# Kernel tuning notes

Hardware: AMD Instinct MI355X
Metric: run time of the kernel (lower is better)

## Reference

```python
import jax, jax.numpy as jnp
import numpy as np

B, S, H = 32, 4096, 512

def setup_inputs() -> dict:
    key = jax.random.key(0)
    k1, k2, k3, k4, k5 = jax.random.split(key, 5)
    scale = 1.0 / np.sqrt(H)
    return {
        "query": jax.random.normal(k1, (B, 1, H), dtype=jnp.float32),
        "keys": jax.random.normal(k2, (B, S, H), dtype=jnp.float32),
        "Wa": jax.random.normal(k3, (H, H), dtype=jnp.float32) * scale,
        "Ua": jax.random.normal(k4, (H, H), dtype=jnp.float32) * scale,
        "Va": jax.random.normal(k5, (H, 1), dtype=jnp.float32) * scale,
    }

def reference(query, keys, Wa, Ua, Va):
    # additive (Bahdanau) attention scores: Va^T tanh(Wa q + Ua k)
    q_proj = jnp.einsum('bqh,hd->bqd', query, Wa)          # [B,1,H]
    k_proj = jnp.einsum('bsh,hd->bsd', keys, Ua)           # [B,S,H]
    scores = jnp.einsum('bsd,d->bs', jnp.tanh(q_proj + k_proj), Va[:, 0])  # [B,S]
    weights = jax.nn.softmax(scores, axis=-1)[:, None, :]  # [B,1,S]
    context = jnp.einsum('bqs,bsh->bqh', weights, keys)    # [B,1,H]
    return (context, weights)
```

## Files before the change

### kernel.cpp

```cpp
#include <hip/hip_runtime.h>
#include <hip/hip_bf16.h>

#define B_ 32
#define S_ 4096
#define H_ 512

typedef short bf16x8 __attribute__((ext_vector_type(8)));
typedef unsigned short u16x8 __attribute__((ext_vector_type(8)));
typedef float f32x4 __attribute__((ext_vector_type(4)));

__device__ inline unsigned short f2bf(float x) {
    unsigned u = __float_as_uint(x);
    return (unsigned short)((u + 0x7fffu + ((u >> 16) & 1u)) >> 16);
}

__device__ inline float fast_tanh(float x) {
    float e = __expf(2.f * x);
    return 1.f - 2.f / (e + 1.f);
}

__device__ __forceinline__ void stage16(const void* g, void* lds_base) {
    __builtin_amdgcn_global_load_lds(
        (const __attribute__((address_space(1))) unsigned char*)g,
        (__attribute__((address_space(3))) unsigned char*)lds_base, 16, 0, 0);
}

__global__ void k_prep_ua(const float* __restrict__ Ua,
                          unsigned short* __restrict__ ua_t) {
    __shared__ float tile[32][33];
    int h0 = blockIdx.x * 32, d0 = blockIdx.y * 32;
    int tx = threadIdx.x, ty = threadIdx.y;
#pragma unroll
    for (int j = 0; j < 4; ++j)
        tile[ty + j * 8][tx] = Ua[(size_t)(h0 + ty + j * 8) * H_ + d0 + tx];
    __syncthreads();
#pragma unroll
    for (int j = 0; j < 4; ++j) {
        int dl = ty + j * 8;
        ua_t[(size_t)(d0 + dl) * H_ + h0 + tx] = f2bf(tile[tx][dl]);
    }
}

__global__ __launch_bounds__(512) void k_qproj(const float* __restrict__ query,
                                               const float* __restrict__ Wa,
                                               float* __restrict__ qproj) {
    __shared__ float q[H_];
    int b = blockIdx.x, d = threadIdx.x;
    q[d] = query[(size_t)b * H_ + d];
    __syncthreads();
    float acc = 0.f;
    for (int h = 0; h < H_; ++h)
        acc = fmaf(q[h], Wa[(size_t)h * H_ + d], acc);
    qproj[(size_t)b * H_ + d] = acc;
}

__global__ __launch_bounds__(256, 3) void k_scores(
    const float* __restrict__ keys, const unsigned short* __restrict__ ua_t,
    const float* __restrict__ qproj, const float* __restrict__ Va,
    float* __restrict__ part_sc) {
    __shared__ __align__(16) unsigned char As[16384];
    __shared__ __align__(16) unsigned char Bs[2][16384];
    __shared__ float smp[2][128];

    int tid = threadIdx.x;
    int wave = tid >> 6, lane = tid & 63;
    int lq = lane & 15, lh = lane >> 4;
    int wm = wave >> 1, wn = wave & 1;

    int logical = (blockIdx.x & 7) * 512 + (blockIdx.x >> 3);
    int b  = logical >> 7;
    int m0 = ((logical >> 2) & 31) * 128;
    int nb = logical & 3;

    const float* keysb = keys + (size_t)b * S_ * H_;

    int r = tid >> 1, hh = tid & 1;
    const float* aptr = keysb + (size_t)(m0 + r) * H_ + hh * 32;
    unsigned aswz = (unsigned)((r & 7) << 4);
    unsigned arow = (unsigned)(r * 128);

    int rbl = lane >> 3;
    unsigned cb = (unsigned)(((lane & 7) * 16) ^ (rbl << 4));
    const unsigned char* uab = (const unsigned char*)ua_t;
    const unsigned char* bsrc[4];
    unsigned bdst[4];
#pragma unroll
    for (int i = 0; i < 4; ++i) {
        int j = wave * 4 + i;
        bsrc[i] = uab + ((size_t)(nb * 128 + 8 * j + rbl)) * 1024 + cb;
        bdst[i] = (unsigned)(j * 1024);
    }

    f32x4 acc[4][4];
#pragma unroll
    for (int i = 0; i < 4; ++i)
#pragma unroll
        for (int j = 0; j < 4; ++j) acc[i][j] = (f32x4){0.f, 0.f, 0.f, 0.f};

#pragma unroll
    for (int i = 0; i < 4; ++i) stage16(bsrc[i], &Bs[0][bdst[i]]);
    {
        float4 a0[8];
#pragma unroll
        for (int j = 0; j < 8; ++j) a0[j] = *(const float4*)(aptr + j * 4);
#pragma unroll
        for (int j16 = 0; j16 < 4; ++j16) {
            float4 x = a0[2 * j16], y = a0[2 * j16 + 1];
            u16x8 v;
            v[0] = f2bf(x.x); v[1] = f2bf(x.y); v[2] = f2bf(x.z); v[3] = f2bf(x.w);
            v[4] = f2bf(y.x); v[5] = f2bf(y.y); v[6] = f2bf(y.z); v[7] = f2bf(y.w);
            *(u16x8*)(As + arow + ((unsigned)(hh * 64 + j16 * 16) ^ aswz)) = v;
        }
    }
    __syncthreads();

#pragma unroll
    for (int t = 0; t < 8; ++t) {
        const int cur = t & 1, nxt = cur ^ 1;
        float4 ar[8];
        if (t < 7) {
#pragma unroll
            for (int i = 0; i < 4; ++i)
                stage16(bsrc[i] + (t + 1) * 128, &Bs[nxt][bdst[i]]);
#pragma unroll
            for (int j = 0; j < 8; ++j)
                ar[j] = *(const float4*)(aptr + (t + 1) * 64 + j * 4);
        }
#pragma unroll
        for (int ks = 0; ks < 2; ++ks) {
            bf16x8 af[4], bv[4];
            unsigned koff = (unsigned)(ks * 64 + lh * 16);
#pragma unroll
            for (int mf = 0; mf < 4; ++mf) {
                unsigned R = (unsigned)(wm * 64 + mf * 16 + lq);
                af[mf] = *(const bf16x8*)(As + R * 128 + (koff ^ ((R & 7) << 4)));
            }
#pragma unroll
            for (int nf = 0; nf < 4; ++nf) {
                unsigned R = (unsigned)(wn * 64 + nf * 16 + lq);
                bv[nf] = *(const bf16x8*)(&Bs[cur][0] + R * 128 + (koff ^ ((R & 7) << 4)));
            }
#pragma unroll
            for (int mf = 0; mf < 4; ++mf)
#pragma unroll
                for (int nf = 0; nf < 4; ++nf)
                    acc[mf][nf] = __builtin_amdgcn_mfma_f32_16x16x32_bf16(
                        af[mf], bv[nf], acc[mf][nf], 0, 0, 0);
        }
        __syncthreads();
        if (t < 7) {
#pragma unroll
            for (int j16 = 0; j16 < 4; ++j16) {
                float4 x = ar[2 * j16], y = ar[2 * j16 + 1];
                u16x8 v;
                v[0] = f2bf(x.x); v[1] = f2bf(x.y); v[2] = f2bf(x.z); v[3] = f2bf(x.w);
                v[4] = f2bf(y.x); v[5] = f2bf(y.y); v[6] = f2bf(y.z); v[7] = f2bf(y.w);
                *(u16x8*)(As + arow + ((unsigned)(hh * 64 + j16 * 16) ^ aswz)) = v;
            }
            __syncthreads();
        }
    }

    float va_r[4], qp_r[4];
#pragma unroll
    for (int nf = 0; nf < 4; ++nf) {
        int n = nb * 128 + wn * 64 + nf * 16 + lq;
        va_r[nf] = Va[n];
        qp_r[nf] = qproj[(size_t)b * H_ + n];
    }
#pragma unroll
    for (int mf = 0; mf < 4; ++mf) {
#pragma unroll
        for (int reg = 0; reg < 4; ++reg) {
            float p = 0.f;
#pragma unroll
            for (int nf = 0; nf < 4; ++nf)
                p += va_r[nf] * fast_tanh(qp_r[nf] + acc[mf][nf][reg]);
            p += __shfl_xor(p, 1);
            p += __shfl_xor(p, 2);
            p += __shfl_xor(p, 4);
            p += __shfl_xor(p, 8);
            if (lq == 0) smp[wn][wm * 64 + mf * 16 + lh * 4 + reg] = p;
        }
    }
    __syncthreads();
    if (tid < 128) {
        float s = smp[0][tid] + smp[1][tid];
        part_sc[((size_t)nb * B_ + b) * S_ + m0 + tid] = s;
    }
}

__global__ __launch_bounds__(512) void k_softmax(const float* __restrict__ part_sc,
                                                 float* __restrict__ wts) {
    __shared__ float red[8];
    int b = blockIdx.x, tid = threadIdx.x;
    const float* p0 = part_sc + (size_t)b * S_;
    const float* p1 = p0 + (size_t)B_ * S_;
    const float* p2 = p1 + (size_t)B_ * S_;
    const float* p3 = p2 + (size_t)B_ * S_;
    float v[8];
    float m = -1e30f;
#pragma unroll
    for (int i = 0; i < 8; ++i) {
        int s = tid + i * 512;
        v[i] = ((p0[s] + p1[s]) + (p2[s] + p3[s]));
        m = fmaxf(m, v[i]);
    }
#pragma unroll
    for (int o = 1; o < 64; o <<= 1) m = fmaxf(m, __shfl_xor(m, o));
    if ((tid & 63) == 0) red[tid >> 6] = m;
    __syncthreads();
    m = red[0];
#pragma unroll
    for (int w = 1; w < 8; ++w) m = fmaxf(m, red[w]);
    float sum = 0.f;
#pragma unroll
    for (int i = 0; i < 8; ++i) {
        v[i] = __expf(v[i] - m);
        sum += v[i];
    }
#pragma unroll
    for (int o = 1; o < 64; o <<= 1) sum += __shfl_xor(sum, o);
    __syncthreads();
    if ((tid & 63) == 0) red[tid >> 6] = sum;
    __syncthreads();
    float tot = 0.f;
#pragma unroll
    for (int w = 0; w < 8; ++w) tot += red[w];
    float inv = 1.f / tot;
#pragma unroll
    for (int i = 0; i < 8; ++i) wts[(size_t)b * S_ + tid + i * 512] = v[i] * inv;
}

__global__ __launch_bounds__(512) void k_ctx_part(const float* __restrict__ keys,
                                                  const float* __restrict__ wts,
                                                  float* __restrict__ part) {
    int c = blockIdx.x, b = blockIdx.y, h = threadIdx.x;
    const float* wrow = wts + (size_t)b * S_ + c * 128;
    const float* kbase = keys + ((size_t)b * S_ + c * 128) * H_ + h;
    float acc = 0.f;
#pragma unroll 8
    for (int s = 0; s < 128; ++s)
        acc = fmaf(wrow[s], kbase[(size_t)s * H_], acc);
    part[((size_t)c * B_ + b) * H_ + h] = acc;
}

__global__ __launch_bounds__(512) void k_ctx_reduce(const float* __restrict__ part,
                                                    float* __restrict__ ctx) {
    int b = blockIdx.x, h = threadIdx.x;
    float s = 0.f;
#pragma unroll
    for (int c = 0; c < 32; ++c) s += part[((size_t)c * B_ + b) * H_ + h];
    ctx[(size_t)b * H_ + h] = s;
}

extern "C" void kernel_launch(void* const* d_in, const int* in_sizes, int n_in,
                              void* d_out, int out_size, void* d_ws, size_t ws_size,
                              hipStream_t stream) {
    const float* query = (const float*)d_in[0];
    const float* keys  = (const float*)d_in[1];
    const float* Wa    = (const float*)d_in[2];
    const float* Ua    = (const float*)d_in[3];
    const float* Va    = (const float*)d_in[4];

    float* out = (float*)d_out;
    float* ctx = out;
    float* wts = out + B_ * H_;

    char* ws = (char*)d_ws;
    unsigned short* ua_t = (unsigned short*)ws;
    float* qproj   = (float*)(ws + 524288);
    float* part_sc = (float*)(ws + 524288 + 65536);
    float* part_cx = (float*)(ws + 524288 + 65536 + 2097152);

    k_prep_ua<<<dim3(16, 16), dim3(32, 8), 0, stream>>>(Ua, ua_t);
    k_qproj<<<dim3(32), dim3(512), 0, stream>>>(query, Wa, qproj);
    k_scores<<<dim3(4096), dim3(256), 0, stream>>>(keys, ua_t, qproj, Va, part_sc);
    k_softmax<<<dim3(32), dim3(512), 0, stream>>>(part_sc, wts);
    k_ctx_part<<<dim3(32, 32), dim3(512), 0, stream>>>(keys, wts, part_cx);
    k_ctx_reduce<<<dim3(32), dim3(512), 0, stream>>>(part_cx, ctx);
}
```

Before: 246.1 us.

## Double-buffer keys tile in LDS and coalesce fp32 key loads

Adds a second LDS buffer for the bf16 keys tile so the next tile is converted and written before the barrier, removing one __syncthreads per k-step. Key loads are remapped so each 16-thread group reads a contiguous 256-byte row segment, and fp32 to bf16 conversion now uses the packed __float22bfloat162_rn intrinsic. The extra 16 KB of LDS lowers the occupancy hint from 3 to 2 blocks per CU, which can reduce latency hiding.

```diff
diff --git a/kernel.cpp b/kernel.cpp
--- a/kernel.cpp
+++ b/kernel.cpp
@@ -6,12 +6,16 @@
 #define H_ 512
 
 typedef short bf16x8 __attribute__((ext_vector_type(8)));
-typedef unsigned short u16x8 __attribute__((ext_vector_type(8)));
 typedef float f32x4 __attribute__((ext_vector_type(4)));
 
 __device__ inline unsigned short f2bf(float x) {
     unsigned u = __float_as_uint(x);
     return (unsigned short)((u + 0x7fffu + ((u >> 16) & 1u)) >> 16);
+}
+
+__device__ __forceinline__ unsigned cvt2(float a, float b) {
+    __hip_bfloat162 h = __float22bfloat162_rn(float2{a, b});
+    return *reinterpret_cast<unsigned*>(&h);
 }
 
 __device__ inline float fast_tanh(float x) {
@@ -54,11 +58,11 @@
     qproj[(size_t)b * H_ + d] = acc;
 }
 
-__global__ __launch_bounds__(256, 3) void k_scores(
+__global__ __launch_bounds__(256, 2) void k_scores(
     const float* __restrict__ keys, const unsigned short* __restrict__ ua_t,
     const float* __restrict__ qproj, const float* __restrict__ Va,
     float* __restrict__ part_sc) {
-    __shared__ __align__(16) unsigned char As[16384];
+    __shared__ __align__(16) unsigned char As[2][16384];
     __shared__ __align__(16) unsigned char Bs[2][16384];
     __shared__ float smp[2][128];
 
@@ -74,20 +78,20 @@
 
     const float* keysb = keys + (size_t)b * S_ * H_;
 
-    int r = tid >> 1, hh = tid & 1;
-    const float* aptr = keysb + (size_t)(m0 + r) * H_ + hh * 32;
-    unsigned aswz = (unsigned)((r & 7) << 4);
-    unsigned arow = (unsigned)(r * 128);
+    int arow_t = tid >> 4;
+    int acolf  = (tid & 15) * 4;
+    const float* aptr = keysb + (size_t)(m0 + arow_t) * H_ + acolf;
+    unsigned awb = (unsigned)(arow_t * 128 + (((tid & 15) * 8) ^ ((arow_t & 7) << 4)));
 
     int rbl = lane >> 3;
-    unsigned cb = (unsigned)(((lane & 7) * 16) ^ (rbl << 4));
+    unsigned cbb = (unsigned)(((lane & 7) * 16) ^ (rbl << 4));
     const unsigned char* uab = (const unsigned char*)ua_t;
     const unsigned char* bsrc[4];
     unsigned bdst[4];
 #pragma unroll
     for (int i = 0; i < 4; ++i) {
         int j = wave * 4 + i;
-        bsrc[i] = uab + ((size_t)(nb * 128 + 8 * j + rbl)) * 1024 + cb;
+        bsrc[i] = uab + ((size_t)(nb * 128 + 8 * j + rbl)) * 1024 + cbb;
         bdst[i] = (unsigned)(j * 1024);
     }
 
@@ -102,14 +106,14 @@
     {
         float4 a0[8];
 #pragma unroll
-        for (int j = 0; j < 8; ++j) a0[j] = *(const float4*)(aptr + j * 4);
-#pragma unroll
-        for (int j16 = 0; j16 < 4; ++j16) {
-            float4 x = a0[2 * j16], y = a0[2 * j16 + 1];
-            u16x8 v;
-            v[0] = f2bf(x.x); v[1] = f2bf(x.y); v[2] = f2bf(x.z); v[3] = f2bf(x.w);
-            v[4] = f2bf(y.x); v[5] = f2bf(y.y); v[6] = f2bf(y.z); v[7] = f2bf(y.w);
-            *(u16x8*)(As + arow + ((unsigned)(hh * 64 + j16 * 16) ^ aswz)) = v;
+        for (int j = 0; j < 8; ++j)
+            a0[j] = *(const float4*)(aptr + (size_t)j * 16 * H_);
+#pragma unroll
+        for (int j = 0; j < 8; ++j) {
+            uint2 w;
+            w.x = cvt2(a0[j].x, a0[j].y);
+            w.y = cvt2(a0[j].z, a0[j].w);
+            *(uint2*)(&As[0][0] + awb + j * 2048) = w;
         }
     }
     __syncthreads();
@@ -124,7 +128,7 @@
                 stage16(bsrc[i] + (t + 1) * 128, &Bs[nxt][bdst[i]]);
 #pragma unroll
             for (int j = 0; j < 8; ++j)
-                ar[j] = *(const float4*)(aptr + (t + 1) * 64 + j * 4);
+                ar[j] = *(const float4*)(aptr + (size_t)j * 16 * H_ + (t + 1) * 64);
         }
 #pragma unroll
         for (int ks = 0; ks < 2; ++ks) {
@@ -133,7 +137,7 @@
 #pragma unroll
             for (int mf = 0; mf < 4; ++mf) {
                 unsigned R = (unsigned)(wm * 64 + mf * 16 + lq);
-                af[mf] = *(const bf16x8*)(As + R * 128 + (koff ^ ((R & 7) << 4)));
+                af[mf] = *(const bf16x8*)(&As[cur][0] + R * 128 + (koff ^ ((R & 7) << 4)));
             }
 #pragma unroll
             for (int nf = 0; nf < 4; ++nf) {
@@ -147,18 +151,16 @@
                     acc[mf][nf] = __builtin_amdgcn_mfma_f32_16x16x32_bf16(
                         af[mf], bv[nf], acc[mf][nf], 0, 0, 0);
         }
+        if (t < 7) {
+#pragma unroll
+            for (int j = 0; j < 8; ++j) {
+                uint2 w;
+                w.x = cvt2(ar[j].x, ar[j].y);
+                w.y = cvt2(ar[j].z, ar[j].w);
+                *(uint2*)(&As[nxt][0] + awb + j * 2048) = w;
+            }
+        }
         __syncthreads();
-        if (t < 7) {
-#pragma unroll
-            for (int j16 = 0; j16 < 4; ++j16) {
-                float4 x = ar[2 * j16], y = ar[2 * j16 + 1];
-                u16x8 v;
-                v[0] = f2bf(x.x); v[1] = f2bf(x.y); v[2] = f2bf(x.z); v[3] = f2bf(x.w);
-                v[4] = f2bf(y.x); v[5] = f2bf(y.y); v[6] = f2bf(y.z); v[7] = f2bf(y.w);
-                *(u16x8*)(As + arow + ((unsigned)(hh * 64 + j16 * 16) ^ aswz)) = v;
-            }
-            __syncthreads();
-        }
     }
 
     float va_r[4], qp_r[4];
```

After: 216.5 us. 1.14x faster.
